# Optimization experiments

Hardware: AMD Instinct MI355X
Metric: run time of the kernel (lower is better)

## Reference

```python
import jax, jax.numpy as jnp
import numpy as np

B, S, D, H = 2, 2048, 2048, 16
HD = D // H  # 128 head dim


def setup_inputs() -> dict:
    key = jax.random.key(0)
    k1, k2, k3 = jax.random.split(key, 3)
    x = jax.random.normal(k1, (B, S, D), dtype=jnp.float32)
    w_qkv = jax.random.normal(k2, (3 * D, D), dtype=jnp.float32) * 0.02
    w_out = jax.random.normal(k3, (D, D), dtype=jnp.float32) * 0.02
    # complex-like RoPE table: freqs_cis[s, j] = exp(i * s * theta^{-2j/hd})
    theta = 10000.0
    inv_freq = 1.0 / (theta ** (jnp.arange(0, HD, 2, dtype=jnp.float32) / HD))  # [HD/2]
    t = jnp.arange(S, dtype=jnp.float32)
    freqs = jnp.outer(t, inv_freq)  # [S, HD/2]
    return {"x": x, "w_qkv": w_qkv, "w_out": w_out,
            "freqs_cos": jnp.cos(freqs), "freqs_sin": jnp.sin(freqs)}


def _apply_rope(t, cos, sin):
    # t: [b, s, h, hd]; adjacent pairs treated as complex (real, imag)
    b, s, h, hd = t.shape
    tr = t.reshape(b, s, h, hd // 2, 2)
    re, im = tr[..., 0], tr[..., 1]
    c = cos[None, :, None, :]  # [1, s, 1, hd/2]
    sn = sin[None, :, None, :]
    out_re = re * c - im * sn
    out_im = re * sn + im * c
    return jnp.stack([out_re, out_im], axis=-1).reshape(b, s, h, hd)


def reference(x, w_qkv, w_out, freqs_cos, freqs_sin):
    b, s, d = x.shape
    qkv = x @ w_qkv.T  # [b, s, 3d]
    q, k, v = jnp.split(qkv, 3, axis=-1)
    q = q.reshape(b, s, H, HD)
    k = k.reshape(b, s, H, HD)
    v = v.reshape(b, s, H, HD)
    q = _apply_rope(q, freqs_cos, freqs_sin)
    k = _apply_rope(k, freqs_cos, freqs_sin)
    # causal SDPA
    scale = 1.0 / jnp.sqrt(jnp.asarray(HD, dtype=x.dtype))
    scores = jnp.einsum("bqhd,bkhd->bhqk", q, k) * scale  # [b, h, s, s]
    causal = jnp.tril(jnp.ones((s, s), dtype=bool))
    scores = jnp.where(causal[None, None], scores, jnp.finfo(scores.dtype).min)
    attn = jax.nn.softmax(scores, axis=-1)
    out = jnp.einsum("bhqk,bkhd->bqhd", attn, v).reshape(b, s, d)
    return out @ w_out.T
```

## Files before the change

kernel.cpp:

```cpp
#include <hip/hip_runtime.h>
#include <hip/hip_bf16.h>
#include <stdint.h>

#define S_ 2048
#define D_ 2048
#define H_ 16
#define HD_ 128

typedef __bf16 bf16x8 __attribute__((ext_vector_type(8)));
typedef float f32x4 __attribute__((ext_vector_type(4)));
typedef unsigned short ushort_t;
typedef ushort_t us4 __attribute__((ext_vector_type(4)));

__device__ __forceinline__ float bf2f(ushort_t u) {
  union { float f; uint32_t i; } x; x.i = ((uint32_t)u) << 16; return x.f;
}
__device__ __forceinline__ ushort_t f2bf(float f) {
  union { float f; uint32_t i; } x; x.f = f;
  uint32_t r = x.i + 0x7fffu + ((x.i >> 16) & 1u);
  return (ushort_t)(r >> 16);
}

__device__ __forceinline__ void async_copy16(const void* g, void* l) {
  __builtin_amdgcn_global_load_lds(
      (const __attribute__((address_space(1))) unsigned int*)g,
      (__attribute__((address_space(3))) unsigned int*)l, 16, 0, 0);
}

__device__ __forceinline__ void store_val(float* p, float v) { *p = v; }
__device__ __forceinline__ void store_val(ushort_t* p, float v) { *p = f2bf(v); }

__global__ __launch_bounds__(256) void cvt_f32_bf16(const float* __restrict__ in,
                                                    ushort_t* __restrict__ out,
                                                    int n4) {
  int i = blockIdx.x * 256 + threadIdx.x;
  if (i >= n4) return;
  const float4 v = ((const float4*)in)[i];
  us4 o;
  o.x = f2bf(v.x); o.y = f2bf(v.y); o.z = f2bf(v.z); o.w = f2bf(v.w);
  ((us4*)out)[i] = o;
}

template <typename OutT>
__global__ __launch_bounds__(256) void gemm_bt(const ushort_t* __restrict__ A,
                                               const ushort_t* __restrict__ Bm,
                                               OutT* __restrict__ C,
                                               int M, int N, int K) {
  __shared__ __align__(16) ushort_t As[128 * 32];
  __shared__ __align__(16) ushort_t Bs[128 * 32];
  const int tid = threadIdx.x;
  const int wave = tid >> 6, lane = tid & 63;
  const int quad = lane >> 4, l16 = lane & 15;
  const int bm = blockIdx.y * 128, bn = blockIdx.x * 128;
  const int wm = (wave >> 1) * 64, wn = (wave & 1) * 64;

  f32x4 acc[4][4] = {};

  const int c0 = wave * 2, c1 = c0 + 1;
  const int srow = lane >> 2;
  const int scol = (lane & 3) * 8;
  const ushort_t* gA0 = A + (size_t)(bm + c0 * 16 + srow) * K + scol;
  const ushort_t* gA1 = A + (size_t)(bm + c1 * 16 + srow) * K + scol;
  const ushort_t* gB0 = Bm + (size_t)(bn + c0 * 16 + srow) * K + scol;
  const ushort_t* gB1 = Bm + (size_t)(bn + c1 * 16 + srow) * K + scol;
  ushort_t* lA0 = As + c0 * 512;
  ushort_t* lA1 = As + c1 * 512;
  ushort_t* lB0 = Bs + c0 * 512;
  ushort_t* lB1 = Bs + c1 * 512;

  for (int k0 = 0; k0 < K; k0 += 32) {
    __syncthreads();
    async_copy16(gA0 + k0, lA0);
    async_copy16(gA1 + k0, lA1);
    async_copy16(gB0 + k0, lB0);
    async_copy16(gB1 + k0, lB1);
    __syncthreads();
    bf16x8 af[4], bfr[4];
#pragma unroll
    for (int i = 0; i < 4; ++i)
      af[i] = *(const bf16x8*)(As + (wm + i * 16 + l16) * 32 + quad * 8);
#pragma unroll
    for (int i = 0; i < 4; ++i)
      bfr[i] = *(const bf16x8*)(Bs + (wn + i * 16 + l16) * 32 + quad * 8);
#pragma unroll
    for (int mi = 0; mi < 4; ++mi)
#pragma unroll
      for (int ni = 0; ni < 4; ++ni)
        acc[mi][ni] = __builtin_amdgcn_mfma_f32_16x16x32_bf16(af[mi], bfr[ni],
                                                              acc[mi][ni], 0, 0, 0);
  }
#pragma unroll
  for (int mi = 0; mi < 4; ++mi)
#pragma unroll
    for (int ni = 0; ni < 4; ++ni)
#pragma unroll
      for (int r = 0; r < 4; ++r) {
        int row = bm + wm + mi * 16 + quad * 4 + r;
        int col = bn + wn + ni * 16 + l16;
        store_val(&C[(size_t)row * N + col], acc[mi][ni][r]);
      }
}

__device__ __forceinline__ void stage_half(const ushort_t* __restrict__ g, int K,
                                           ushort_t* l, int wave, int srow,
                                           int clog) {
#pragma unroll
  for (int i = 0; i < 2; ++i)
    async_copy16(g + (size_t)(i * 64 + srow) * K + clog * 8,
                 l + wave * 512 + i * 4096);
}

#define MFMA_BF16(a, b, c) __builtin_amdgcn_mfma_f32_16x16x32_bf16(a, b, c, 0, 0, 0)

template <typename OutT>
__global__ __launch_bounds__(512, 2) void gemm_bt256(const ushort_t* __restrict__ A,
                                                     const ushort_t* __restrict__ Bm,
                                                     OutT* __restrict__ C,
                                                     int M, int N, int K) {
  __shared__ __align__(16) ushort_t As[2][256 * 64];
  __shared__ __align__(16) ushort_t Bs[2][256 * 64];
  const int tid = threadIdx.x;
  const int wave = tid >> 6, lane = tid & 63;
  const int quad = lane >> 4, l16 = lane & 15;
  const int bm = blockIdx.y * 256, bn = blockIdx.x * 256;
  const int wm = (wave >> 2) * 128;
  const int wn = (wave & 3) * 64;
  const int srow = tid >> 3;
  const int clog = (tid & 7) ^ (srow & 7);
  const int ck0 = (quad ^ (l16 & 7)) * 8;
  const int ck1 = ((4 + quad) ^ (l16 & 7)) * 8;

  const ushort_t* gA = A + (size_t)bm * K;
  const ushort_t* gB = Bm + (size_t)bn * K;
  const int NT = K >> 6;

  f32x4 acc[8][4] = {};

  stage_half(gA, K, &As[0][0], wave, srow, clog);
  stage_half(gA + (size_t)128 * K, K, &As[0][8192], wave, srow, clog);
  stage_half(gB, K, &Bs[0][0], wave, srow, clog);
  stage_half(gB + (size_t)128 * K, K, &Bs[0][8192], wave, srow, clog);
  if (NT > 1) {
    stage_half(gA + 64, K, &As[1][0], wave, srow, clog);
    asm volatile("s_waitcnt vmcnt(2)" ::: "memory");
  } else {
    asm volatile("s_waitcnt vmcnt(0)" ::: "memory");
  }
  __builtin_amdgcn_sched_barrier(0);
  __builtin_amdgcn_s_barrier();

  for (int t = 0; t < NT; ++t) {
    const ushort_t* A_cur = &As[t & 1][0];
    const ushort_t* B_cur = &Bs[t & 1][0];
    ushort_t* A_nxt = &As[(t + 1) & 1][0];
    ushort_t* B_nxt = &Bs[(t + 1) & 1][0];
    const ushort_t* Arow = A_cur + (wm + l16) * 64;
    const ushort_t* Brow = B_cur + (wn + l16) * 64;
    const size_t kn = (size_t)(t + 1) * 64;
    const bool pf1 = (t + 1 < NT);
    const bool pf2 = (t + 2 < NT);

    bf16x8 a4[4][2], b01[2][2], b23[2][2];

#pragma unroll
    for (int mi = 0; mi < 4; ++mi) {
      a4[mi][0] = *(const bf16x8*)(Arow + mi * 1024 + ck0);
      a4[mi][1] = *(const bf16x8*)(Arow + mi * 1024 + ck1);
    }
#pragma unroll
    for (int ni = 0; ni < 2; ++ni) {
      b01[ni][0] = *(const bf16x8*)(Brow + ni * 1024 + ck0);
      b01[ni][1] = *(const bf16x8*)(Brow + ni * 1024 + ck1);
    }
    if (pf1) stage_half(gA + (size_t)128 * K + kn, K, A_nxt + 8192, wave, srow, clog);
    __builtin_amdgcn_s_barrier();
    __builtin_amdgcn_s_setprio(1);
#pragma unroll
    for (int mi = 0; mi < 4; ++mi)
#pragma unroll
      for (int ni = 0; ni < 2; ++ni) {
        acc[mi][ni] = MFMA_BF16(a4[mi][0], b01[ni][0], acc[mi][ni]);
        acc[mi][ni] = MFMA_BF16(a4[mi][1], b01[ni][1], acc[mi][ni]);
      }
    __builtin_amdgcn_s_setprio(0);
    __builtin_amdgcn_s_barrier();

#pragma unroll
    for (int ni = 0; ni < 2; ++ni) {
      b23[ni][0] = *(const bf16x8*)(Brow + (ni + 2) * 1024 + ck0);
      b23[ni][1] = *(const bf16x8*)(Brow + (ni + 2) * 1024 + ck1);
    }
    if (pf1) stage_half(gB + kn, K, B_nxt, wave, srow, clog);
    __builtin_amdgcn_s_barrier();
    __builtin_amdgcn_s_setprio(1);
#pragma unroll
    for (int mi = 0; mi < 4; ++mi)
#pragma unroll
      for (int ni = 0; ni < 2; ++ni) {
        acc[mi][ni + 2] = MFMA_BF16(a4[mi][0], b23[ni][0], acc[mi][ni + 2]);
        acc[mi][ni + 2] = MFMA_BF16(a4[mi][1], b23[ni][1], acc[mi][ni + 2]);
      }
    __builtin_amdgcn_s_setprio(0);
    __builtin_amdgcn_s_barrier();

#pragma unroll
    for (int mi = 0; mi < 4; ++mi) {
      a4[mi][0] = *(const bf16x8*)(Arow + (mi + 4) * 1024 + ck0);
      a4[mi][1] = *(const bf16x8*)(Arow + (mi + 4) * 1024 + ck1);
    }
    if (pf1) stage_half(gB + (size_t)128 * K + kn, K, B_nxt + 8192, wave, srow, clog);
    __builtin_amdgcn_s_barrier();
    __builtin_amdgcn_s_setprio(1);
#pragma unroll
    for (int mi = 0; mi < 4; ++mi)
#pragma unroll
      for (int ni = 0; ni < 2; ++ni) {
        acc[mi + 4][ni] = MFMA_BF16(a4[mi][0], b01[ni][0], acc[mi + 4][ni]);
        acc[mi + 4][ni] = MFMA_BF16(a4[mi][1], b01[ni][1], acc[mi + 4][ni]);
      }
    __builtin_amdgcn_s_setprio(0);
    __builtin_amdgcn_s_barrier();

    if (pf2) {
      stage_half(gA + (size_t)(t + 2) * 64, K, (ushort_t*)A_cur, wave, srow, clog);
      asm volatile("s_waitcnt vmcnt(2)" ::: "memory");
    } else {
      asm volatile("s_waitcnt vmcnt(0)" ::: "memory");
    }
    __builtin_amdgcn_sched_barrier(0);
    __builtin_amdgcn_s_barrier();
    __builtin_amdgcn_s_setprio(1);
#pragma unroll
    for (int mi = 0; mi < 4; ++mi)
#pragma unroll
      for (int ni = 0; ni < 2; ++ni) {
        acc[mi + 4][ni + 2] = MFMA_BF16(a4[mi][0], b23[ni][0], acc[mi + 4][ni + 2]);
        acc[mi + 4][ni + 2] = MFMA_BF16(a4[mi][1], b23[ni][1], acc[mi + 4][ni + 2]);
      }
    __builtin_amdgcn_s_setprio(0);
    __builtin_amdgcn_s_barrier();
    __builtin_amdgcn_sched_barrier(0);
  }

#pragma unroll
  for (int mi = 0; mi < 8; ++mi)
#pragma unroll
    for (int ni = 0; ni < 4; ++ni)
#pragma unroll
      for (int r = 0; r < 4; ++r) {
        int row = bm + wm + mi * 16 + quad * 4 + r;
        int col = bn + wn + ni * 16 + l16;
        store_val(&C[(size_t)row * N + col], acc[mi][ni][r]);
      }
}

__global__ __launch_bounds__(256) void rope_k(ushort_t* __restrict__ qkv,
                                              const float* __restrict__ fc,
                                              const float* __restrict__ fs) {
  int idx = blockIdx.x * 256 + threadIdx.x;
  int i = idx & 63;
  int hh = (idx >> 6) & 15;
  int m = idx >> 10;
  int s = m & (S_ - 1);
  float c = fc[s * 64 + i], sn = fs[s * 64 + i];
  size_t off = (size_t)m * (3 * D_) + hh * HD_ + 2 * i;
#pragma unroll
  for (int part = 0; part < 2; ++part) {
    uint32_t* p = (uint32_t*)(qkv + off + part * D_);
    uint32_t v = *p;
    float re = bf2f((ushort_t)(v & 0xffffu));
    float im = bf2f((ushort_t)(v >> 16));
    float nr = re * c - im * sn;
    float ni = re * sn + im * c;
    *p = (uint32_t)f2bf(nr) | ((uint32_t)f2bf(ni) << 16);
  }
}

__global__ __launch_bounds__(256) void vt_prep(const ushort_t* __restrict__ qkv,
                                               ushort_t* __restrict__ VTg) {
  __shared__ __align__(16) ushort_t T[64 * 136];
  const int st = blockIdx.x, h = blockIdx.y, b = blockIdx.z;
  const int tid = threadIdx.x;
  const ushort_t* gV = qkv + (size_t)(b * S_ + st * 64) * (3 * D_) + 2 * D_ + h * HD_;
  {
    const int r = tid >> 2, cc = (tid & 3) * 32;
    const ushort_t* src = gV + (size_t)r * (3 * D_) + cc;
    uint4 a0 = ((const uint4*)src)[0];
    uint4 a1 = ((const uint4*)src)[1];
    uint4 a2 = ((const uint4*)src)[2];
    uint4 a3 = ((const uint4*)src)[3];
    ushort_t* dst = T + r * 136 + cc;
    ((uint4*)dst)[0] = a0; ((uint4*)dst)[1] = a1;
    ((uint4*)dst)[2] = a2; ((uint4*)dst)[3] = a3;
  }
  __syncthreads();
  const int d = tid >> 1, kh = (tid & 1) * 32;
  ushort_t buf[32];
#pragma unroll
  for (int j = 0; j < 32; ++j) buf[j] = T[(kh + j) * 136 + d];
  ushort_t* out = VTg + ((size_t)((b * H_ + h) * HD_ + d)) * S_ + st * 64 + kh;
  ((uint4*)out)[0] = *(const uint4*)(buf + 0);
  ((uint4*)out)[1] = *(const uint4*)(buf + 8);
  ((uint4*)out)[2] = *(const uint4*)(buf + 16);
  ((uint4*)out)[3] = *(const uint4*)(buf + 24);
}

#define SOFTMAX_C 12.0f

__global__ __launch_bounds__(256, 4) void attn_fwd(const ushort_t* __restrict__ qkv,
                                                   const ushort_t* __restrict__ VTg,
                                                   float* __restrict__ Oacc,
                                                   float* __restrict__ lsum_g) {
  __shared__ __align__(16) ushort_t Kl[64 * 128];
  __shared__ __align__(16) ushort_t VT[128 * 64];
  __shared__ __align__(16) ushort_t Pl[4 * 16 * 64];

  const int j = 79 - (int)blockIdx.x;
  int qt, c;
  if (j < 8)       { qt = j;                 c = 0; }
  else if (j < 24) { int t = j - 8;  qt = 8 + (t >> 1);  c = t & 1; }
  else if (j < 48) { int t = j - 24; qt = 16 + t / 3;    c = t % 3; }
  else             { int t = j - 48; qt = 24 + (t >> 2); c = t & 3; }
  const int h = blockIdx.y, b = blockIdx.z;
  const int kt0 = c * 8;
  const int kt_end = min(kt0 + 8, qt + 1);

  const int tid = threadIdx.x;
  const int wave = tid >> 6, lane = tid & 63;
  const int quad = lane >> 4, l16 = lane & 15;
  const float scale = 0.08838834764831845f;

  const int qg = qt * 64 + wave * 16 + l16;
  const ushort_t* qrow = qkv + (size_t)(b * S_ + qg) * (3 * D_) + h * HD_;
  bf16x8 qf[4];
#pragma unroll
  for (int cc = 0; cc < 4; ++cc)
    qf[cc] = *(const bf16x8*)(qrow + cc * 32 + quad * 8);

  f32x4 o[8] = {};
  float lsum[4] = {0.f, 0.f, 0.f, 0.f};
  const int q_row_base = qt * 64 + wave * 16 + quad * 4;
  ushort_t* Pw = Pl + wave * 16 * 64;

  const ushort_t* gK = qkv + (size_t)(b * S_) * (3 * D_) + D_ + h * HD_;
  const ushort_t* gVT = VTg + (size_t)(b * H_ + h) * HD_ * S_;

  const int krow_off = lane >> 4;
  const int kchunk = lane & 15;
  const int vrow_off = lane >> 3;
  const int vchunk = lane & 7;

  for (int kt = kt0; kt < kt_end; ++kt) {
    __syncthreads();
#pragma unroll
    for (int i = 0; i < 4; ++i) {
      int row = wave * 16 + i * 4 + krow_off;
      int lchunk = kchunk ^ (row & 15);
      async_copy16(gK + (size_t)(kt * 64 + row) * (3 * D_) + lchunk * 8,
                   Kl + (wave * 16 + i * 4) * 128);
    }
#pragma unroll
    for (int i = 0; i < 4; ++i) {
      int row = wave * 32 + i * 8 + vrow_off;
      int lchunk = vchunk ^ (row & 7);
      async_copy16(gVT + (size_t)row * S_ + kt * 64 + lchunk * 8,
                   VT + (wave * 32 + i * 8) * 64);
    }
    __syncthreads();

    const bool diag = (kt == qt);
#pragma unroll
    for (int g = 0; g < 4; ++g) {
      f32x4 s = {0.f, 0.f, 0.f, 0.f};
#pragma unroll
      for (int cc = 0; cc < 4; ++cc) {
        bf16x8 kf = *(const bf16x8*)(Kl + (g * 16 + l16) * 128 +
                                     (((cc * 4 + quad) ^ l16) * 8));
        s = __builtin_amdgcn_mfma_f32_16x16x32_bf16(qf[cc], kf, s, 0, 0, 0);
      }
      const int key = kt * 64 + g * 16 + l16;
#pragma unroll
      for (int r = 0; r < 4; ++r) {
        float e = __expf(s[r] * scale - SOFTMAX_C);
        float p = (!diag || key <= q_row_base + r) ? e : 0.f;
        lsum[r] += p;
        int prow = quad * 4 + r;
        int pcol = g * 16 + l16;
        Pw[prow * 64 + (((pcol >> 3) ^ (prow & 7)) * 8) + (pcol & 7)] = f2bf(p);
      }
    }
    bf16x8 pf0 = *(const bf16x8*)(Pw + l16 * 64 + ((quad ^ (l16 & 7)) * 8));
    bf16x8 pf1 = *(const bf16x8*)(Pw + l16 * 64 + (((4 + quad) ^ (l16 & 7)) * 8));
#pragma unroll
    for (int dc = 0; dc < 8; ++dc) {
      bf16x8 v0 = *(const bf16x8*)(VT + (dc * 16 + l16) * 64 +
                                   (((0 * 4 + quad) ^ (l16 & 7)) * 8));
      o[dc] = __builtin_amdgcn_mfma_f32_16x16x32_bf16(pf0, v0, o[dc], 0, 0, 0);
      bf16x8 v1 = *(const bf16x8*)(VT + (dc * 16 + l16) * 64 +
                                   (((1 * 4 + quad) ^ (l16 & 7)) * 8));
      o[dc] = __builtin_amdgcn_mfma_f32_16x16x32_bf16(pf1, v1, o[dc], 0, 0, 0);
    }
  }

#pragma unroll
  for (int r = 0; r < 4; ++r) {
    float l = lsum[r];
    l += __shfl_xor(l, 1, 64);
    l += __shfl_xor(l, 2, 64);
    l += __shfl_xor(l, 4, 64);
    l += __shfl_xor(l, 8, 64);
    size_t row = (size_t)(b * S_ + q_row_base + r);
    if (l16 == 0) unsafeAtomicAdd(&lsum_g[row * H_ + h], l);
#pragma unroll
    for (int dc = 0; dc < 8; ++dc)
      unsafeAtomicAdd(&Oacc[row * D_ + h * HD_ + dc * 16 + l16], o[dc][r]);
  }
}

__global__ __launch_bounds__(256) void combine(const float* __restrict__ Oacc,
                                               const float* __restrict__ lsum_g,
                                               ushort_t* __restrict__ attn) {
  int i = blockIdx.x * 256 + threadIdx.x;
  float4 v = ((const float4*)Oacc)[i];
  int flat = i * 4;
  int row = flat >> 11;
  int h = (flat >> 7) & 15;
  float inv = 1.0f / lsum_g[row * H_ + h];
  us4 o;
  o.x = f2bf(v.x * inv); o.y = f2bf(v.y * inv);
  o.z = f2bf(v.z * inv); o.w = f2bf(v.w * inv);
  ((us4*)attn)[i] = o;
}

extern "C" void kernel_launch(void* const* d_in, const int* in_sizes, int n_in,
                              void* d_out, int out_size, void* d_ws, size_t ws_size,
                              hipStream_t stream) {
  const float* x = (const float*)d_in[0];
  const float* w_qkv = (const float*)d_in[1];
  const float* w_out = (const float*)d_in[2];
  const float* fcos = (const float*)d_in[3];
  const float* fsin = (const float*)d_in[4];
  float* out = (float*)d_out;

  char* ws = (char*)d_ws;
  ushort_t* x_bf    = (ushort_t*)(ws + 0);
  ushort_t* wqkv_bf = (ushort_t*)(ws + 16777216);
  ushort_t* wout_bf = (ushort_t*)(ws + 41943040);
  ushort_t* qkv     = (ushort_t*)(ws + 50331648);
  ushort_t* attn    = (ushort_t*)(ws + 100663296);
  float* Oacc   = (float*)(ws + 0);
  float* lsum_g = (float*)(ws + 33554432);
  ushort_t* VTg = (ushort_t*)(ws + 100663296);

  cvt_f32_bf16<<<8192, 256, 0, stream>>>(x, x_bf, 2097152);
  cvt_f32_bf16<<<12288, 256, 0, stream>>>(w_qkv, wqkv_bf, 3145728);
  cvt_f32_bf16<<<4096, 256, 0, stream>>>(w_out, wout_bf, 1048576);

  gemm_bt256<ushort_t><<<dim3(24, 16), 512, 0, stream>>>(x_bf, wqkv_bf, qkv,
                                                         4096, 6144, 2048);
  rope_k<<<16384, 256, 0, stream>>>(qkv, fcos, fsin);
  vt_prep<<<dim3(32, 16, 2), 256, 0, stream>>>(qkv, VTg);

  hipMemsetAsync(Oacc, 0, 33554432, stream);
  hipMemsetAsync(lsum_g, 0, 262144, stream);

  attn_fwd<<<dim3(80, 16, 2), 256, 0, stream>>>(qkv, VTg, Oacc, lsum_g);
  combine<<<8192, 256, 0, stream>>>(Oacc, lsum_g, attn);

  gemm_bt<float><<<dim3(16, 32), 256, 0, stream>>>(attn, wout_bf, out,
                                                   4096, 2048, 2048);
}
```

Before: 453.9 us.

## Prefetch GEMM tiles two k-steps ahead and interleave MFMA chains by k-slice

The GEMM main loop now issues global-to-LDS loads for tile t+2 into the buffer being consumed, replacing the old one-step-ahead staggered prefetch. The prologue stages both k-tiles up front, and the waitcnt thresholds change to match. The MFMA loops are reordered so the two k-halves form independent chains across accumulators, which reduces back-to-back dependence on a single accumulator. The aim is to hide more global latency, at the cost of relying on barriers so buffers aren't overwritten while still being read.

```diff
diff --git a/kernel.cpp b/kernel.cpp
--- a/kernel.cpp
+++ b/kernel.cpp
@@ -142,7 +142,10 @@
   stage_half(gB + (size_t)128 * K, K, &Bs[0][8192], wave, srow, clog);
   if (NT > 1) {
     stage_half(gA + 64, K, &As[1][0], wave, srow, clog);
-    asm volatile("s_waitcnt vmcnt(2)" ::: "memory");
+    stage_half(gA + (size_t)128 * K + 64, K, &As[1][8192], wave, srow, clog);
+    stage_half(gB + 64, K, &Bs[1][0], wave, srow, clog);
+    stage_half(gB + (size_t)128 * K + 64, K, &Bs[1][8192], wave, srow, clog);
+    asm volatile("s_waitcnt vmcnt(8)" ::: "memory");
   } else {
     asm volatile("s_waitcnt vmcnt(0)" ::: "memory");
   }
@@ -150,14 +153,11 @@
   __builtin_amdgcn_s_barrier();
 
   for (int t = 0; t < NT; ++t) {
-    const ushort_t* A_cur = &As[t & 1][0];
-    const ushort_t* B_cur = &Bs[t & 1][0];
-    ushort_t* A_nxt = &As[(t + 1) & 1][0];
-    ushort_t* B_nxt = &Bs[(t + 1) & 1][0];
+    ushort_t* A_cur = &As[t & 1][0];
+    ushort_t* B_cur = &Bs[t & 1][0];
     const ushort_t* Arow = A_cur + (wm + l16) * 64;
     const ushort_t* Brow = B_cur + (wn + l16) * 64;
-    const size_t kn = (size_t)(t + 1) * 64;
-    const bool pf1 = (t + 1 < NT);
+    const size_t kn2 = (size_t)(t + 2) * 64;
     const bool pf2 = (t + 2 < NT);
 
     bf16x8 a4[4][2], b01[2][2], b23[2][2];
@@ -172,16 +172,15 @@
       b01[ni][0] = *(const bf16x8*)(Brow + ni * 1024 + ck0);
       b01[ni][1] = *(const bf16x8*)(Brow + ni * 1024 + ck1);
     }
-    if (pf1) stage_half(gA + (size_t)128 * K + kn, K, A_nxt + 8192, wave, srow, clog);
     __builtin_amdgcn_s_barrier();
     __builtin_amdgcn_s_setprio(1);
 #pragma unroll
-    for (int mi = 0; mi < 4; ++mi)
-#pragma unroll
-      for (int ni = 0; ni < 2; ++ni) {
-        acc[mi][ni] = MFMA_BF16(a4[mi][0], b01[ni][0], acc[mi][ni]);
-        acc[mi][ni] = MFMA_BF16(a4[mi][1], b01[ni][1], acc[mi][ni]);
-      }
+    for (int ks = 0; ks < 2; ++ks)
+#pragma unroll
+      for (int mi = 0; mi < 4; ++mi)
+#pragma unroll
+        for (int ni = 0; ni < 2; ++ni)
+          acc[mi][ni] = MFMA_BF16(a4[mi][ks], b01[ni][ks], acc[mi][ni]);
     __builtin_amdgcn_s_setprio(0);
     __builtin_amdgcn_s_barrier();
 
@@ -190,16 +189,15 @@
       b23[ni][0] = *(const bf16x8*)(Brow + (ni + 2) * 1024 + ck0);
       b23[ni][1] = *(const bf16x8*)(Brow + (ni + 2) * 1024 + ck1);
     }
-    if (pf1) stage_half(gB + kn, K, B_nxt, wave, srow, clog);
     __builtin_amdgcn_s_barrier();
     __builtin_amdgcn_s_setprio(1);
 #pragma unroll
-    for (int mi = 0; mi < 4; ++mi)
-#pragma unroll
-      for (int ni = 0; ni < 2; ++ni) {
-        acc[mi][ni + 2] = MFMA_BF16(a4[mi][0], b23[ni][0], acc[mi][ni + 2]);
-        acc[mi][ni + 2] = MFMA_BF16(a4[mi][1], b23[ni][1], acc[mi][ni + 2]);
-      }
+    for (int ks = 0; ks < 2; ++ks)
+#pragma unroll
+      for (int mi = 0; mi < 4; ++mi)
+#pragma unroll
+        for (int ni = 0; ni < 2; ++ni)
+          acc[mi][ni + 2] = MFMA_BF16(a4[mi][ks], b23[ni][ks], acc[mi][ni + 2]);
     __builtin_amdgcn_s_setprio(0);
     __builtin_amdgcn_s_barrier();
 
@@ -208,22 +206,26 @@
       a4[mi][0] = *(const bf16x8*)(Arow + (mi + 4) * 1024 + ck0);
       a4[mi][1] = *(const bf16x8*)(Arow + (mi + 4) * 1024 + ck1);
     }
-    if (pf1) stage_half(gB + (size_t)128 * K + kn, K, B_nxt + 8192, wave, srow, clog);
+    if (pf2) {
+      stage_half(gB + kn2, K, B_cur, wave, srow, clog);
+      stage_half(gB + (size_t)128 * K + kn2, K, B_cur + 8192, wave, srow, clog);
+    }
     __builtin_amdgcn_s_barrier();
     __builtin_amdgcn_s_setprio(1);
 #pragma unroll
-    for (int mi = 0; mi < 4; ++mi)
-#pragma unroll
-      for (int ni = 0; ni < 2; ++ni) {
-        acc[mi + 4][ni] = MFMA_BF16(a4[mi][0], b01[ni][0], acc[mi + 4][ni]);
-        acc[mi + 4][ni] = MFMA_BF16(a4[mi][1], b01[ni][1], acc[mi + 4][ni]);
-      }
+    for (int ks = 0; ks < 2; ++ks)
+#pragma unroll
+      for (int mi = 0; mi < 4; ++mi)
+#pragma unroll
+        for (int ni = 0; ni < 2; ++ni)
+          acc[mi + 4][ni] = MFMA_BF16(a4[mi][ks], b01[ni][ks], acc[mi + 4][ni]);
     __builtin_amdgcn_s_setprio(0);
     __builtin_amdgcn_s_barrier();
 
     if (pf2) {
-      stage_half(gA + (size_t)(t + 2) * 64, K, (ushort_t*)A_cur, wave, srow, clog);
-      asm volatile("s_waitcnt vmcnt(2)" ::: "memory");
+      stage_half(gA + kn2, K, A_cur, wave, srow, clog);
+      stage_half(gA + (size_t)128 * K + kn2, K, A_cur + 8192, wave, srow, clog);
+      asm volatile("s_waitcnt vmcnt(8)" ::: "memory");
     } else {
       asm volatile("s_waitcnt vmcnt(0)" ::: "memory");
     }
@@ -231,12 +233,12 @@
     __builtin_amdgcn_s_barrier();
     __builtin_amdgcn_s_setprio(1);
 #pragma unroll
-    for (int mi = 0; mi < 4; ++mi)
-#pragma unroll
-      for (int ni = 0; ni < 2; ++ni) {
-        acc[mi + 4][ni + 2] = MFMA_BF16(a4[mi][0], b23[ni][0], acc[mi + 4][ni + 2]);
-        acc[mi + 4][ni + 2] = MFMA_BF16(a4[mi][1], b23[ni][1], acc[mi + 4][ni + 2]);
-      }
+    for (int ks = 0; ks < 2; ++ks)
+#pragma unroll
+      for (int mi = 0; mi < 4; ++mi)
+#pragma unroll
+        for (int ni = 0; ni < 2; ++ni)
+          acc[mi + 4][ni + 2] = MFMA_BF16(a4[mi][ks], b23[ni][ks], acc[mi + 4][ni + 2]);
     __builtin_amdgcn_s_setprio(0);
     __builtin_amdgcn_s_barrier();
     __builtin_amdgcn_sched_barrier(0);
```

Result: no change. 460.9 us (+1.5%).
